# Optimization experiments

Measured on AMD Instinct MI355X. Metric: run time of the kernel, lower is better.

## Reference

```python
import jax, jax.numpy as jnp
import numpy as np

BATCH = 2048
TEMP = 0.5

def setup_inputs() -> dict:
    key = jax.random.key(0)
    k1, k2 = jax.random.split(key)
    z1 = jax.random.normal(k1, (BATCH, 1024), dtype=jnp.float32)
    z2 = jax.random.normal(k2, (BATCH, 1024), dtype=jnp.float32)
    return {"z1": z1, "z2": z2}

def _l2norm(x, eps=1e-12):
    # matches F.normalize(dim=1): x / max(||x||, eps)
    n = jnp.sqrt(jnp.sum(x * x, axis=1, keepdims=True))
    return x / jnp.maximum(n, eps)

def reference(z1, z2):
    B = z1.shape[0]
    z1n = _l2norm(z1)
    z2n = _l2norm(z2)
    z = jnp.concatenate([z1n, z2n], axis=0)  # [2B, C], unit-norm rows
    # cosine_similarity of unit vectors == dot product -> single GEMM
    S = z @ z.T  # [2B, 2B]
    # positives: S[i, i+B] for i<B and S[i, i-B] for i>=B
    pos_upper = jnp.diagonal(S, offset=B)   # [B]
    pos_lower = jnp.diagonal(S, offset=-B)  # [B]
    positives = jnp.concatenate([pos_upper, pos_lower], axis=0)  # [2B]
    neg_mask = 1.0 - jnp.eye(2 * B, dtype=S.dtype)
    den = jnp.sum(neg_mask * jnp.exp(S / TEMP), axis=1)  # [2B]
    loss = -jnp.mean(positives / TEMP - jnp.log(den))
    return loss
```

## Files before the change

### kernel.cpp

```cpp
#include <hip/hip_runtime.h>
#include <hip/hip_bf16.h>

#define NROW 4096
#define HALFB 2048
#define CDIM 1024
#define INV_T 2.0f
#define NBLK 32
#define NTRI 528
#define NT 8

typedef __attribute__((ext_vector_type(4))) float f32x4;
typedef __attribute__((ext_vector_type(8))) int i32x8;

__global__ __launch_bounds__(256) void normalize_kernel(
        const float* __restrict__ z1, const float* __restrict__ z2,
        unsigned int* __restrict__ zb8, float* __restrict__ den) {
    const int row = blockIdx.x;
    const int t = threadIdx.x;
    if (row < 16) den[row * 256 + t] = 0.f;
    const float* src = (row < HALFB) ? (z1 + (size_t)row * CDIM)
                                     : (z2 + (size_t)(row - HALFB) * CDIM);
    float4 v = ((const float4*)src)[t];
    float ss = v.x * v.x + v.y * v.y + v.z * v.z + v.w * v.w;
    #pragma unroll
    for (int off = 1; off < 64; off <<= 1) ss += __shfl_xor(ss, off);
    __shared__ float wsum[4];
    const int lane = t & 63, wv = t >> 6;
    if (lane == 0) wsum[wv] = ss;
    __syncthreads();
    const float tot = wsum[0] + wsum[1] + wsum[2] + wsum[3];
    const float scale = 1.0f / fmaxf(sqrtf(tot), 1e-12f);
    int w = __builtin_amdgcn_cvt_pk_fp8_f32(v.x * scale, v.y * scale, 0, false);
    w = __builtin_amdgcn_cvt_pk_fp8_f32(v.z * scale, v.w * scale, w, true);
    zb8[(size_t)row * 256 + t] = (unsigned int)w;
}

__global__ __launch_bounds__(256) void gemm_den_kernel(
        const unsigned char* __restrict__ zb8, float* __restrict__ den,
        float* __restrict__ pos) {
    __shared__ __align__(16) unsigned char As[128 * 128];
    __shared__ __align__(16) unsigned char Bs[128 * 128];

    const int orig = blockIdx.x;
    int swz = (orig & 7) * (NTRI / 8) + (orig >> 3);
    int bi = 0, rem = swz;
    while (rem >= NBLK - bi) { rem -= NBLK - bi; ++bi; }
    const int bj = bi + rem;
    const int i0 = bi * 128, j0 = bj * 128;
    const bool diag = (bi == bj);
    const bool is_pos = (bj == bi + 16);

    const int tid = threadIdx.x;
    const int wave = tid >> 6, lane = tid & 63;
    const int wr = wave >> 1, wc = wave & 1;

    f32x4 acc[4][4];
    #pragma unroll
    for (int m = 0; m < 4; m++)
        #pragma unroll
        for (int n = 0; n < 4; n++) acc[m][n] = (f32x4){0.f, 0.f, 0.f, 0.f};

    const int srow = lane >> 3;
    const int schunk = (lane & 7) ^ srow;

    const int l15 = lane & 15, ks = lane >> 4;

    for (int t = 0; t < NT; ++t) {
        const int kb = t * 128;
        #pragma unroll
        for (int c = 0; c < 4; ++c) {
            const int r0 = (wave * 4 + c) * 8;
            const unsigned char* ga =
                zb8 + (size_t)(i0 + r0 + srow) * CDIM + kb + schunk * 16;
            __builtin_amdgcn_global_load_lds(
                (const __attribute__((address_space(1))) void*)ga,
                (__attribute__((address_space(3))) void*)(As + r0 * 128),
                16, 0, 0);
            const unsigned char* gb =
                zb8 + (size_t)(j0 + r0 + srow) * CDIM + kb + schunk * 16;
            __builtin_amdgcn_global_load_lds(
                (const __attribute__((address_space(1))) void*)gb,
                (__attribute__((address_space(3))) void*)(Bs + r0 * 128),
                16, 0, 0);
        }
        __syncthreads();

        i32x8 b[4];
        #pragma unroll
        for (int n = 0; n < 4; ++n) {
            const int r = wc * 64 + n * 16 + l15;
            const int c0 = (2 * ks) ^ (r & 7);
            const int c1 = (2 * ks + 1) ^ (r & 7);
            const int4 lo = *(const int4*)(Bs + r * 128 + c0 * 16);
            const int4 hi = *(const int4*)(Bs + r * 128 + c1 * 16);
            b[n] = (i32x8){lo.x, lo.y, lo.z, lo.w, hi.x, hi.y, hi.z, hi.w};
        }
        __builtin_amdgcn_s_setprio(1);
        #pragma unroll
        for (int m = 0; m < 4; ++m) {
            const int r = wr * 64 + m * 16 + l15;
            const int c0 = (2 * ks) ^ (r & 7);
            const int c1 = (2 * ks + 1) ^ (r & 7);
            const int4 lo = *(const int4*)(As + r * 128 + c0 * 16);
            const int4 hi = *(const int4*)(As + r * 128 + c1 * 16);
            const i32x8 a = (i32x8){lo.x, lo.y, lo.z, lo.w, hi.x, hi.y, hi.z, hi.w};
            #pragma unroll
            for (int n = 0; n < 4; ++n)
                acc[m][n] = __builtin_amdgcn_mfma_scale_f32_16x16x128_f8f6f4(
                    a, b[n], acc[m][n],
                    0 , 0 ,
                    0, 127 ,
                    0, 127 );
        }
        __builtin_amdgcn_s_setprio(0);
        __syncthreads();
    }

    if (is_pos && wr == wc) {
        #pragma unroll
        for (int m = 0; m < 4; ++m) {
            #pragma unroll
            for (int r = 0; r < 4; ++r) {
                if (l15 == ks * 4 + r)
                    pos[i0 + wr * 64 + m * 16 + l15] = acc[m][m][r];
            }
        }
    }

    float cs[4] = {0.f, 0.f, 0.f, 0.f};
    #pragma unroll
    for (int m = 0; m < 4; ++m) {
        #pragma unroll
        for (int r = 0; r < 4; ++r) {
            float rs = 0.f;
            #pragma unroll
            for (int n = 0; n < 4; ++n) {
                const float e = __expf(INV_T * acc[m][n][r]);
                rs += e;
                cs[n] += e;
            }
            rs += __shfl_xor(rs, 1);
            rs += __shfl_xor(rs, 2);
            rs += __shfl_xor(rs, 4);
            rs += __shfl_xor(rs, 8);
            if (l15 == 0) {
                const int grow = i0 + wr * 64 + m * 16 + ks * 4 + r;
                atomicAdd(&den[grow], rs);
            }
        }
    }
    if (!diag) {
        #pragma unroll
        for (int n = 0; n < 4; ++n) {
            float c = cs[n];
            c += __shfl_xor(c, 16);
            c += __shfl_xor(c, 32);
            if (lane < 16) {
                const int gcol = j0 + wc * 64 + n * 16 + lane;
                atomicAdd(&den[gcol], c);
            }
        }
    }
}

__global__ __launch_bounds__(256) void loss_kernel(
        const float* __restrict__ den, const float* __restrict__ pos,
        float* __restrict__ out) {
    const float E2 = 7.3890560989306495f;
    const int tid = threadIdx.x;
    float acc = 0.f;
    for (int i = tid; i < NROW; i += 256)
        acc += INV_T * pos[i & (HALFB - 1)] - logf(den[i] - E2);
    #pragma unroll
    for (int off = 1; off < 64; off <<= 1) acc += __shfl_xor(acc, off);
    __shared__ float wsum[4];
    const int lane = tid & 63, wv = tid >> 6;
    if (lane == 0) wsum[wv] = acc;
    __syncthreads();
    if (tid == 0) out[0] = -(wsum[0] + wsum[1] + wsum[2] + wsum[3]) * (1.0f / NROW);
}

extern "C" void kernel_launch(void* const* d_in, const int* in_sizes, int n_in,
                              void* d_out, int out_size, void* d_ws, size_t ws_size,
                              hipStream_t stream) {
    const float* z1 = (const float*)d_in[0];
    const float* z2 = (const float*)d_in[1];
    float* out = (float*)d_out;

    unsigned int* zb8 = (unsigned int*)d_ws;
    float* den = (float*)((char*)d_ws + (size_t)NROW * CDIM);
    float* pos = den + NROW;

    normalize_kernel<<<NROW, 256, 0, stream>>>(z1, z2, zb8, den);
    gemm_den_kernel<<<NTRI, 256, 0, stream>>>((const unsigned char*)zb8, den, pos);
    loss_kernel<<<1, 256, 0, stream>>>(den, pos, out);
}
```

Measured before the change: 35.78 us.

## Quantize normalized embeddings to FP4 and use FP4 scaled MFMA

Normalized rows are encoded as FP4 (E2M1) with a fixed power-of-two block scale, replacing FP8, which halves operand bytes and LDS tiles. The GEMM uses the f8f6f4 scaled MFMA in FP4 mode with E8M0 scales to undo the ×32 prescale. This cuts global and LDS traffic and may raise MFMA throughput, but it adds a software encoder and a large loss of precision that could break the accuracy tolerance.

```diff
diff --git a/kernel.cpp b/kernel.cpp
--- a/kernel.cpp
+++ b/kernel.cpp
@@ -8,13 +8,33 @@
 #define NBLK 32
 #define NTRI 528
 #define NT 8
+#define RB 512
+#define SCALE_E8M0 122
 
 typedef __attribute__((ext_vector_type(4))) float f32x4;
 typedef __attribute__((ext_vector_type(8))) int i32x8;
 
+__device__ __forceinline__ unsigned enc_fp4(float q) {
+    const unsigned s = q < 0.f ? 8u : 0u;
+    const float a = fabsf(q);
+    unsigned m;
+    if (a < 1.25f) {
+        if (a < 0.25f)      m = 0;
+        else if (a < 0.75f) m = 1;
+        else                m = 2;
+    } else if (a < 2.5f) {
+        m = (a < 1.75f) ? 3u : 4u;
+    } else {
+        if (a < 3.5f)       m = 5;
+        else if (a < 5.0f)  m = 6;
+        else                m = 7;
+    }
+    return s | m;
+}
+
 __global__ __launch_bounds__(256) void normalize_kernel(
         const float* __restrict__ z1, const float* __restrict__ z2,
-        unsigned int* __restrict__ zb8, float* __restrict__ den) {
+        unsigned short* __restrict__ zb4, float* __restrict__ den) {
     const int row = blockIdx.x;
     const int t = threadIdx.x;
     if (row < 16) den[row * 256 + t] = 0.f;
@@ -29,17 +49,19 @@
     if (lane == 0) wsum[wv] = ss;
     __syncthreads();
     const float tot = wsum[0] + wsum[1] + wsum[2] + wsum[3];
-    const float scale = 1.0f / fmaxf(sqrtf(tot), 1e-12f);
-    int w = __builtin_amdgcn_cvt_pk_fp8_f32(v.x * scale, v.y * scale, 0, false);
-    w = __builtin_amdgcn_cvt_pk_fp8_f32(v.z * scale, v.w * scale, w, true);
-    zb8[(size_t)row * 256 + t] = (unsigned int)w;
+    const float scale = 32.0f / fmaxf(sqrtf(tot), 1e-12f);
+    const unsigned c0 = enc_fp4(v.x * scale);
+    const unsigned c1 = enc_fp4(v.y * scale);
+    const unsigned c2 = enc_fp4(v.z * scale);
+    const unsigned c3 = enc_fp4(v.w * scale);
+    zb4[(size_t)row * 256 + t] = (unsigned short)(c0 | (c1 << 4) | (c2 << 8) | (c3 << 12));
 }
 
 __global__ __launch_bounds__(256) void gemm_den_kernel(
-        const unsigned char* __restrict__ zb8, float* __restrict__ den,
+        const unsigned char* __restrict__ zb4, float* __restrict__ den,
         float* __restrict__ pos) {
-    __shared__ __align__(16) unsigned char As[128 * 128];
-    __shared__ __align__(16) unsigned char Bs[128 * 128];
+    __shared__ __align__(16) unsigned char As[128 * 64];
+    __shared__ __align__(16) unsigned char Bs[128 * 64];
 
     const int orig = blockIdx.x;
     int swz = (orig & 7) * (NTRI / 8) + (orig >> 3);
@@ -60,27 +82,27 @@
         #pragma unroll
         for (int n = 0; n < 4; n++) acc[m][n] = (f32x4){0.f, 0.f, 0.f, 0.f};
 
-    const int srow = lane >> 3;
-    const int schunk = (lane & 7) ^ srow;
+    const int srow = lane >> 2;
+    const int schunk = (lane & 3) ^ ((srow >> 1) & 3);
 
     const int l15 = lane & 15, ks = lane >> 4;
 
     for (int t = 0; t < NT; ++t) {
-        const int kb = t * 128;
-        #pragma unroll
-        for (int c = 0; c < 4; ++c) {
-            const int r0 = (wave * 4 + c) * 8;
+        const int kb = t * 64;
+        #pragma unroll
+        for (int c = 0; c < 2; ++c) {
+            const int r0 = wave * 32 + c * 16;
             const unsigned char* ga =
-                zb8 + (size_t)(i0 + r0 + srow) * CDIM + kb + schunk * 16;
+                zb4 + (size_t)(i0 + r0 + srow) * RB + kb + schunk * 16;
             __builtin_amdgcn_global_load_lds(
                 (const __attribute__((address_space(1))) void*)ga,
-                (__attribute__((address_space(3))) void*)(As + r0 * 128),
+                (__attribute__((address_space(3))) void*)(As + r0 * 64),
                 16, 0, 0);
             const unsigned char* gb =
-                zb8 + (size_t)(j0 + r0 + srow) * CDIM + kb + schunk * 16;
+                zb4 + (size_t)(j0 + r0 + srow) * RB + kb + schunk * 16;
             __builtin_amdgcn_global_load_lds(
                 (const __attribute__((address_space(1))) void*)gb,
-                (__attribute__((address_space(3))) void*)(Bs + r0 * 128),
+                (__attribute__((address_space(3))) void*)(Bs + r0 * 64),
                 16, 0, 0);
         }
         __syncthreads();
@@ -89,28 +111,24 @@
         #pragma unroll
         for (int n = 0; n < 4; ++n) {
             const int r = wc * 64 + n * 16 + l15;
-            const int c0 = (2 * ks) ^ (r & 7);
-            const int c1 = (2 * ks + 1) ^ (r & 7);
-            const int4 lo = *(const int4*)(Bs + r * 128 + c0 * 16);
-            const int4 hi = *(const int4*)(Bs + r * 128 + c1 * 16);
-            b[n] = (i32x8){lo.x, lo.y, lo.z, lo.w, hi.x, hi.y, hi.z, hi.w};
+            const int slot = ks ^ ((r >> 1) & 3);
+            const int4 w = *(const int4*)(Bs + r * 64 + slot * 16);
+            b[n] = (i32x8){w.x, w.y, w.z, w.w, 0, 0, 0, 0};
         }
         __builtin_amdgcn_s_setprio(1);
         #pragma unroll
         for (int m = 0; m < 4; ++m) {
             const int r = wr * 64 + m * 16 + l15;
-            const int c0 = (2 * ks) ^ (r & 7);
-            const int c1 = (2 * ks + 1) ^ (r & 7);
-            const int4 lo = *(const int4*)(As + r * 128 + c0 * 16);
-            const int4 hi = *(const int4*)(As + r * 128 + c1 * 16);
-            const i32x8 a = (i32x8){lo.x, lo.y, lo.z, lo.w, hi.x, hi.y, hi.z, hi.w};
+            const int slot = ks ^ ((r >> 1) & 3);
+            const int4 w = *(const int4*)(As + r * 64 + slot * 16);
+            const i32x8 a = (i32x8){w.x, w.y, w.z, w.w, 0, 0, 0, 0};
             #pragma unroll
             for (int n = 0; n < 4; ++n)
                 acc[m][n] = __builtin_amdgcn_mfma_scale_f32_16x16x128_f8f6f4(
                     a, b[n], acc[m][n],
-                    0 , 0 ,
-                    0, 127 ,
-                    0, 127 );
+                    4 , 4 ,
+                    0, SCALE_E8M0 ,
+                    0, SCALE_E8M0 );
         }
         __builtin_amdgcn_s_setprio(0);
         __syncthreads();
@@ -187,11 +205,11 @@
     const float* z2 = (const float*)d_in[1];
     float* out = (float*)d_out;
 
-    unsigned int* zb8 = (unsigned int*)d_ws;
-    float* den = (float*)((char*)d_ws + (size_t)NROW * CDIM);
+    unsigned short* zb4 = (unsigned short*)d_ws;
+    float* den = (float*)((char*)d_ws + (size_t)NROW * RB);
     float* pos = den + NROW;
 
-    normalize_kernel<<<NROW, 256, 0, stream>>>(z1, z2, zb8, den);
-    gemm_den_kernel<<<NTRI, 256, 0, stream>>>((const unsigned char*)zb8, den, pos);
+    normalize_kernel<<<NROW, 256, 0, stream>>>(z1, z2, zb4, den);
+    gemm_den_kernel<<<NTRI, 256, 0, stream>>>((const unsigned char*)zb4, den, pos);
     loss_kernel<<<1, 256, 0, stream>>>(den, pos, out);
 }
```

Result: faster. 33.21 us (-7.2%).
